# Optimization experiments

Measured on AMD Instinct MI355X. Metric: run time of the kernel, lower is better.

The kernel has to match this reference:

```python
import jax, jax.numpy as jnp
import numpy as np

S, B, L, V, D, T, G = 16, 8, 8, 32000, 1024, 512, 3


def setup_inputs() -> dict:
    key = jax.random.key(0)
    k = jax.random.split(key, 10)
    s = 0.05
    return {
        "encoded_hidden": jax.random.normal(k[0], (B, D), jnp.float32),
        "encoded_outputs": jax.random.normal(k[1], (B, T, D), jnp.float32),
        "story": jax.random.randint(k[2], (B, T), 0, V),
        "trg_batches": jax.random.randint(k[3], (B, S, L), 0, V),
        "embedding": jax.random.normal(k[4], (V, D), jnp.float32) * 0.1,
        "w_ih": jax.random.normal(k[5], (3 * D, D), jnp.float32) * s,
        "w_hh": jax.random.normal(k[6], (3 * D, D), jnp.float32) * s,
        "b_ih": jnp.zeros((3 * D,), jnp.float32),
        "b_hh": jnp.zeros((3 * D,), jnp.float32),
        "w_ratio_w": jax.random.normal(k[7], (1, 3 * D), jnp.float32) * s,
        "w_ratio_b": jnp.zeros((1,), jnp.float32),
        "w_gate_w": jax.random.normal(k[8], (G, D), jnp.float32) * s,
        "w_gate_b": jnp.zeros((G,), jnp.float32),
        "slot_emb": jax.random.normal(k[9], (S, D), jnp.float32) * 0.1,
    }


def reference(encoded_hidden, encoded_outputs, story, trg_batches, embedding,
              w_ih, w_hh, b_ih, b_hh, w_ratio_w, w_ratio_b,
              w_gate_w, w_gate_b, slot_emb):
    # Decoder inputs per (slot, step): step 0 = slot embedding,
    # step i>0 = embedding of teacher-forced target token i-1.  -> x: (S,L,B,D)
    x0 = jnp.broadcast_to(slot_emb[:, None, None, :], (S, 1, B, D))
    xt = jnp.transpose(embedding[trg_batches[:, :, :L - 1]], (1, 2, 0, 3))  # (S,L-1,B,D)
    x = jnp.concatenate([x0, xt], axis=1)

    # Single GRU step; hidden is reset to the encoder hidden each step (as in source),
    # so decoder_state == new hidden and all (slot,step) cells are independent.
    h0 = encoded_hidden  # (B,D)
    gi = jnp.einsum('slbd,ed->slbe', x, w_ih) + b_ih          # (S,L,B,3D)
    gh = h0 @ w_hh.T + b_hh                                    # (B,3D)
    ir, iz, inn = jnp.split(gi, 3, axis=-1)
    hr, hz, hn = jnp.split(gh, 3, axis=-1)
    r = jax.nn.sigmoid(ir + hr)
    z = jax.nn.sigmoid(iz + hz)
    n = jnp.tanh(inn + r * hn)
    h = (1.0 - z) * n + z * h0                                 # (S,L,B,D)

    # History attention; NOTE: context uses the RAW scores (source quirk).
    scores = jnp.einsum('slbd,btd->slbt', h, encoded_outputs)  # (S,L,B,T)
    probs = jax.nn.softmax(scores, axis=-1)
    context = jnp.einsum('slbt,btd->slbd', scores, encoded_outputs)

    # Vocab distribution p_vocab = softmax(h @ E^T)
    p_vocab = jax.nn.softmax(jnp.einsum('slbd,vd->slbv', h, embedding), axis=-1)

    # Pointer-generator gate
    feat = jnp.concatenate([h, context, x], axis=-1)           # (S,L,B,3D)
    p_gen = jax.nn.sigmoid(jnp.einsum('slbe,oe->slbo', feat, w_ratio_w) + w_ratio_b)  # (S,L,B,1)

    # Copy distribution via scatter-add of attention probs onto vocab ids
    def scatter_one(p_b, story_b):  # p_b: (S,L,T), story_b: (T,)
        return jnp.zeros((S, L, V), p_b.dtype).at[:, :, story_b].add(p_b)
    p_ctx = jax.vmap(scatter_one, in_axes=(2, 0), out_axes=2)(probs, story)  # (S,L,B,V)

    p_final = p_gen * p_vocab + (1.0 - p_gen) * p_ctx
    ptr_outputs = jnp.transpose(p_final, (0, 2, 1, 3))         # (S,B,L,V)
    gate_outputs = context[:, 0] @ w_gate_w.T + w_gate_b       # (S,B,G), from step 0
    return ptr_outputs, gate_outputs
```

## Files before the change

### kernel.cpp

```cpp
#include <hip/hip_runtime.h>

#define S_ 16
#define B_ 8
#define L_ 8
#define V_ 32000
#define D_ 1024
#define T_ 512
#define G_ 3
#define M_ 1024
#define E3_ 3072

typedef unsigned short U16;
typedef __attribute__((ext_vector_type(8))) short short8;
typedef __attribute__((ext_vector_type(4))) float f32x4;

__device__ __forceinline__ U16 f2bf(float f) {
  union { float f; unsigned u; } c; c.f = f;
  unsigned u = c.u;
  return (U16)((u + 0x7FFFu + ((u >> 16) & 1u)) >> 16);
}
__device__ __forceinline__ float bf2f(U16 h) {
  union { unsigned u; float f; } c; c.u = ((unsigned)h) << 16;
  return c.f;
}
__device__ __forceinline__ void split2(float f, U16& hi, U16& lo) {
  hi = f2bf(f);
  lo = f2bf(f - bf2f(hi));
}

__global__ void k_cast_emb(const float* __restrict__ emb, U16* __restrict__ emb_bf) {
  int idx = blockIdx.x * 256 + threadIdx.x;
  float4 v = ((const float4*)emb)[idx];
  ushort4 o;
  o.x = f2bf(v.x); o.y = f2bf(v.y); o.z = f2bf(v.z); o.w = f2bf(v.w);
  ((ushort4*)emb_bf)[idx] = o;
}

__global__ void k_cast_wih(const float* __restrict__ w, U16* __restrict__ wh, U16* __restrict__ wl) {
  int idx = blockIdx.x * 256 + threadIdx.x;
  float4 v = ((const float4*)w)[idx];
  ushort4 h4, l4;
  split2(v.x, h4.x, l4.x); split2(v.y, h4.y, l4.y);
  split2(v.z, h4.z, l4.z); split2(v.w, h4.w, l4.w);
  ((ushort4*)wh)[idx] = h4;
  ((ushort4*)wl)[idx] = l4;
}

__global__ void k_cast_enc(const float* __restrict__ enc,
                           U16* __restrict__ enc_h, U16* __restrict__ enc_l,
                           U16* __restrict__ encT_h, U16* __restrict__ encT_l) {
  __shared__ U16 hs[32][36];
  __shared__ U16 ls[32][36];
  int b = blockIdx.z, t0 = blockIdx.x * 32, d0 = blockIdx.y * 32;
  int r  = threadIdx.x >> 3;
  int c4 = (threadIdx.x & 7) * 4;
  size_t src_idx = ((size_t)(b * T_ + t0 + r)) * D_ + d0 + c4;
  float4 v = *(const float4*)(enc + src_idx);
  ushort4 h4, l4;
  split2(v.x, h4.x, l4.x); split2(v.y, h4.y, l4.y);
  split2(v.z, h4.z, l4.z); split2(v.w, h4.w, l4.w);
  *(ushort4*)(enc_h + src_idx) = h4;
  *(ushort4*)(enc_l + src_idx) = l4;
  hs[r][c4+0] = h4.x; hs[r][c4+1] = h4.y; hs[r][c4+2] = h4.z; hs[r][c4+3] = h4.w;
  ls[r][c4+0] = l4.x; ls[r][c4+1] = l4.y; ls[r][c4+2] = l4.z; ls[r][c4+3] = l4.w;
  __syncthreads();
  ushort4 th, tl;
  th.x = hs[c4+0][r]; th.y = hs[c4+1][r]; th.z = hs[c4+2][r]; th.w = hs[c4+3][r];
  tl.x = ls[c4+0][r]; tl.y = ls[c4+1][r]; tl.z = ls[c4+2][r]; tl.w = ls[c4+3][r];
  size_t dst_idx = ((size_t)(b * D_ + d0 + r)) * T_ + t0 + c4;
  *(ushort4*)(encT_h + dst_idx) = th;
  *(ushort4*)(encT_l + dst_idx) = tl;
}

__global__ void k_build_x(const float* __restrict__ emb, const float* __restrict__ slot_emb,
                          const int* __restrict__ trg, float* __restrict__ x,
                          U16* __restrict__ x_h, U16* __restrict__ x_l) {
  int m = blockIdx.x;
  int d = threadIdx.x * 4;
  int b = m >> 7, s = (m >> 3) & 15, l = m & 7;
  const float* src;
  if (l == 0) src = slot_emb + s * D_;
  else        src = emb + (size_t)trg[b * (S_ * L_) + s * L_ + (l - 1)] * D_;
  float4 v = *(const float4*)(src + d);
  *(float4*)(x + (size_t)m * D_ + d) = v;
  ushort4 h4, l4;
  split2(v.x, h4.x, l4.x); split2(v.y, h4.y, l4.y);
  split2(v.z, h4.z, l4.z); split2(v.w, h4.w, l4.w);
  *(ushort4*)(x_h + (size_t)m * D_ + d) = h4;
  *(ushort4*)(x_l + (size_t)m * D_ + d) = l4;
}

__global__ void k_gh(const float* __restrict__ h0, const float* __restrict__ w_hh,
                     const float* __restrict__ b_hh, float* __restrict__ gh) {
  int b = blockIdx.y;
  int e = blockIdx.x * 64 + (threadIdx.x >> 2);
  int part = threadIdx.x & 3;
  const float* hr = h0 + b * D_ + part * 256;
  const float* wr = w_hh + (size_t)e * D_ + part * 256;
  float s = 0.f;
  for (int i = 0; i < 256; ++i) s += hr[i] * wr[i];
  s += __shfl_xor(s, 1);
  s += __shfl_xor(s, 2);
  if (part == 0) gh[b * E3_ + e] = s + b_hh[e];
}

__device__ __forceinline__ void stage_tile(U16* __restrict__ sm, const U16* __restrict__ g,
                                           int row0, int k0, int lda, int tid) {
#pragma unroll
  for (int i = 0; i < 2; ++i) {
    int o = (i * 256 + tid) * 16;
    int row = o >> 6;
    int chunk = ((o >> 4) & 3) ^ ((row >> 1) & 3);
    const U16* gp = g + (size_t)(row0 + row) * lda + k0 + chunk * 8;
    U16* sp = sm + (o >> 1);
    __builtin_amdgcn_global_load_lds((const __attribute__((address_space(1))) unsigned int*)gp,
                                     (__attribute__((address_space(3))) unsigned int*)sp,
                                     16, 0, 0);
  }
}

__device__ __forceinline__ short8 frag_ld(const U16* __restrict__ sm, int rowbase, int ln) {
  int row = rowbase + (ln & 15);
  int chunk = (ln >> 4) ^ ((row >> 1) & 3);
  return *(const short8*)(sm + row * 32 + chunk * 8);
}

template <bool HILO, bool VOCAB>
__global__ __launch_bounds__(256, 2)
void k_gemm(const U16* __restrict__ Ah, const U16* __restrict__ Al,
            const U16* __restrict__ Bh, const U16* __restrict__ Bl,
            float* __restrict__ C, float* __restrict__ rowsum,
            int Ktot, int lda, int ldb, int ldc,
            long sA, long sB, long sC) {
  __shared__ U16 smem[(HILO ? 4 : 2) * 128 * 32];
  U16* Ash = smem;
  U16* Bsh = smem + 4096;
  U16* Asl = HILO ? (smem + 8192) : smem;
  U16* Bsl = HILO ? (smem + 12288) : smem;

  int tid = threadIdx.x;
  int ln = tid & 63, w = tid >> 6;
  int wr = (w >> 1) * 64, wc = (w & 1) * 64;
  int n0 = blockIdx.x * 128, m0 = blockIdx.y * 128;
  int bz = blockIdx.z;
  const U16* pAh = Ah + (size_t)bz * sA;
  const U16* pBh = Bh + (size_t)bz * sB;
  const U16* pAl = HILO ? (Al + (size_t)bz * sA) : nullptr;
  const U16* pBl = HILO ? (Bl + (size_t)bz * sB) : nullptr;

  f32x4 acc[4][4];
#pragma unroll
  for (int i = 0; i < 4; i++)
#pragma unroll
    for (int j = 0; j < 4; j++) acc[i][j] = (f32x4)(0.f);

  for (int k0 = 0; k0 < Ktot; k0 += 32) {
    __syncthreads();
    stage_tile(Ash, pAh, m0, k0, lda, tid);
    stage_tile(Bsh, pBh, n0, k0, ldb, tid);
    if constexpr (HILO) {
      stage_tile(Asl, pAl, m0, k0, lda, tid);
      stage_tile(Bsl, pBl, n0, k0, ldb, tid);
    }
    __syncthreads();

    short8 a_h[4], b_h[4];
#pragma unroll
    for (int i = 0; i < 4; i++) {
      a_h[i] = frag_ld(Ash, wr + i * 16, ln);
      b_h[i] = frag_ld(Bsh, wc + i * 16, ln);
    }
    if constexpr (HILO) {
      short8 a_l[4], b_l[4];
#pragma unroll
      for (int i = 0; i < 4; i++) {
        a_l[i] = frag_ld(Asl, wr + i * 16, ln);
        b_l[i] = frag_ld(Bsl, wc + i * 16, ln);
      }
#pragma unroll
      for (int i = 0; i < 4; i++)
#pragma unroll
        for (int j = 0; j < 4; j++) {
          acc[i][j] = __builtin_amdgcn_mfma_f32_16x16x32_bf16(a_h[i], b_h[j], acc[i][j], 0, 0, 0);
          acc[i][j] = __builtin_amdgcn_mfma_f32_16x16x32_bf16(a_h[i], b_l[j], acc[i][j], 0, 0, 0);
          acc[i][j] = __builtin_amdgcn_mfma_f32_16x16x32_bf16(a_l[i], b_h[j], acc[i][j], 0, 0, 0);
        }
    } else {
#pragma unroll
      for (int i = 0; i < 4; i++)
#pragma unroll
        for (int j = 0; j < 4; j++)
          acc[i][j] = __builtin_amdgcn_mfma_f32_16x16x32_bf16(a_h[i], b_h[j], acc[i][j], 0, 0, 0);
    }
  }

  int quad = ln >> 4, col = ln & 15;
  if constexpr (!VOCAB) {
    float* pC = C + (size_t)bz * sC;
#pragma unroll
    for (int i = 0; i < 4; i++)
#pragma unroll
      for (int j = 0; j < 4; j++)
#pragma unroll
        for (int r = 0; r < 4; r++)
          pC[(size_t)(m0 + wr + i * 16 + quad * 4 + r) * ldc + (n0 + wc + j * 16 + col)] =
              acc[i][j][r];
  } else {
#pragma unroll
    for (int i = 0; i < 4; i++)
#pragma unroll
      for (int r = 0; r < 4; r++) {
        int m = m0 + wr + i * 16 + quad * 4 + r;
        int s_ = (m >> 3) & 15, l_ = m & 7, b_ = m >> 7;
        size_t obase = (size_t)((s_ * B_ + b_) * L_ + l_) * (size_t)V_;
        float rs = 0.f;
#pragma unroll
        for (int j = 0; j < 4; j++) {
          float e = __expf(acc[i][j][r]);
          C[obase + (n0 + wc + j * 16 + col)] = e;
          rs += e;
        }
        rs += __shfl_xor(rs, 1);
        rs += __shfl_xor(rs, 2);
        rs += __shfl_xor(rs, 4);
        rs += __shfl_xor(rs, 8);
        if (col == 0) atomicAdd(&rowsum[m], rs);
      }
  }
}

__global__ void k_h(const float* __restrict__ gi, const float* __restrict__ gh,
                    const float* __restrict__ h0, const float* __restrict__ b_ih,
                    float* __restrict__ h, U16* __restrict__ h_h, U16* __restrict__ h_l) {
  int m = blockIdx.x;
  int d = threadIdx.x * 4;
  int b = m >> 7;
  float4 ir  = *(const float4*)(gi + (size_t)m * E3_ + d);
  float4 iz  = *(const float4*)(gi + (size_t)m * E3_ + D_ + d);
  float4 in_ = *(const float4*)(gi + (size_t)m * E3_ + 2 * D_ + d);
  float4 bir = *(const float4*)(b_ih + d);
  float4 biz = *(const float4*)(b_ih + D_ + d);
  float4 bin = *(const float4*)(b_ih + 2 * D_ + d);
  float4 hr  = *(const float4*)(gh + b * E3_ + d);
  float4 hz  = *(const float4*)(gh + b * E3_ + D_ + d);
  float4 hn  = *(const float4*)(gh + b * E3_ + 2 * D_ + d);
  float4 h0v = *(const float4*)(h0 + b * D_ + d);
  float4 out;
#define GRU1(c)                                             \
  {                                                         \
    float rr = 1.f / (1.f + __expf(-(ir.c + bir.c + hr.c))); \
    float zz = 1.f / (1.f + __expf(-(iz.c + biz.c + hz.c))); \
    float nn = tanhf(in_.c + bin.c + rr * hn.c);            \
    out.c = (1.f - zz) * nn + zz * h0v.c;                   \
  }
  GRU1(x) GRU1(y) GRU1(z) GRU1(w)
#undef GRU1
  *(float4*)(h + (size_t)m * D_ + d) = out;
  ushort4 h4, l4;
  split2(out.x, h4.x, l4.x); split2(out.y, h4.y, l4.y);
  split2(out.z, h4.z, l4.z); split2(out.w, h4.w, l4.w);
  *(ushort4*)(h_h + (size_t)m * D_ + d) = h4;
  *(ushort4*)(h_l + (size_t)m * D_ + d) = l4;
}

__global__ void k_softmax(const float* __restrict__ scores, float* __restrict__ probs,
                          U16* __restrict__ s_h, U16* __restrict__ s_l) {
  int m = blockIdx.x;
  int tid = threadIdx.x;
  int ln = tid & 63, w = tid >> 6;
  float v0 = scores[(size_t)m * T_ + tid];
  float v1 = scores[(size_t)m * T_ + 256 + tid];
  U16 hh, ll;
  split2(v0, hh, ll); s_h[m * T_ + tid] = hh;       s_l[m * T_ + tid] = ll;
  split2(v1, hh, ll); s_h[m * T_ + 256 + tid] = hh; s_l[m * T_ + 256 + tid] = ll;
  float mx = fmaxf(v0, v1);
#pragma unroll
  for (int msk = 32; msk >= 1; msk >>= 1) mx = fmaxf(mx, __shfl_xor(mx, msk));
  __shared__ float red[4];
  if (ln == 0) red[w] = mx;
  __syncthreads();
  mx = fmaxf(fmaxf(red[0], red[1]), fmaxf(red[2], red[3]));
  float e0 = __expf(v0 - mx), e1 = __expf(v1 - mx);
  float sm = e0 + e1;
#pragma unroll
  for (int msk = 32; msk >= 1; msk >>= 1) sm += __shfl_xor(sm, msk);
  __syncthreads();
  if (ln == 0) red[w] = sm;
  __syncthreads();
  float inv = 1.f / (red[0] + red[1] + red[2] + red[3]);
  probs[(size_t)m * T_ + tid] = e0 * inv;
  probs[(size_t)m * T_ + 256 + tid] = e1 * inv;
}

__global__ void k_pgen(const float* __restrict__ h, const float* __restrict__ ctx,
                       const float* __restrict__ x, const float* __restrict__ wr,
                       const float* __restrict__ wrb, float* __restrict__ p_gen,
                       float* __restrict__ rowsum) {
  int m = blockIdx.x;
  int tid = threadIdx.x;
  int ln = tid & 63, w = tid >> 6;
  float sacc = 0.f;
  for (int j = tid; j < D_; j += 256)
    sacc += h[(size_t)m * D_ + j] * wr[j] + ctx[(size_t)m * D_ + j] * wr[D_ + j] +
            x[(size_t)m * D_ + j] * wr[2 * D_ + j];
#pragma unroll
  for (int msk = 32; msk >= 1; msk >>= 1) sacc += __shfl_xor(sacc, msk);
  __shared__ float red[4];
  if (ln == 0) red[w] = sacc;
  __syncthreads();
  if (tid == 0) {
    float t = red[0] + red[1] + red[2] + red[3] + wrb[0];
    p_gen[m] = 1.f / (1.f + expf(-t));
    rowsum[m] = 0.f;
  }
}

__global__ void k_gate(const float* __restrict__ ctx, const float* __restrict__ wg,
                       const float* __restrict__ wgb, float* __restrict__ out_gate) {
  int id = blockIdx.x;
  int g = id % 3;
  int sb = id / 3;
  int b = sb & 7, s = sb >> 3;
  int m = (b * S_ + s) * L_;
  int ln = threadIdx.x;
  float acc = 0.f;
  for (int d = ln; d < D_; d += 64) acc += ctx[(size_t)m * D_ + d] * wg[g * D_ + d];
#pragma unroll
  for (int msk = 32; msk >= 1; msk >>= 1) acc += __shfl_xor(acc, msk);
  if (ln == 0) out_gate[id] = acc + wgb[g];
}

__global__ void k_scale(float* __restrict__ out, const float* __restrict__ p_gen,
                        const float* __restrict__ rowsum) {
  int idx = blockIdx.x * 256 + threadIdx.x;
  int osl = idx / (V_ / 4);
  int s = osl >> 6, b = (osl >> 3) & 7, l = osl & 7;
  int m = (b << 7) | (s << 3) | l;
  float sc = p_gen[m] / rowsum[m];
  float4* p = (float4*)out + idx;
  float4 v = *p;
  v.x *= sc; v.y *= sc; v.z *= sc; v.w *= sc;
  *p = v;
}

__global__ void k_scatter(float* __restrict__ out, const float* __restrict__ p_gen,
                          const float* __restrict__ probs, const int* __restrict__ story) {
  int id = blockIdx.x * 256 + threadIdx.x;
  int m = id >> 9, t = id & 511;
  int b = m >> 7, s = (m >> 3) & 15, l = m & 7;
  float val = (1.f - p_gen[m]) * probs[(size_t)m * T_ + t];
  int v = story[b * T_ + t];
  size_t o = (size_t)((s * B_ + b) * L_ + l) * (size_t)V_ + v;
  atomicAdd(out + o, val);
}

extern "C" void kernel_launch(void* const* d_in, const int* in_sizes, int n_in,
                              void* d_out, int out_size, void* d_ws, size_t ws_size,
                              hipStream_t stream) {
  (void)in_sizes; (void)n_in; (void)out_size; (void)ws_size;
  const float* enc_hid   = (const float*)d_in[0];
  const float* enc_out   = (const float*)d_in[1];
  const int*   story     = (const int*)d_in[2];
  const int*   trg       = (const int*)d_in[3];
  const float* emb       = (const float*)d_in[4];
  const float* w_ih      = (const float*)d_in[5];
  const float* w_hh      = (const float*)d_in[6];
  const float* b_ih      = (const float*)d_in[7];
  const float* b_hh      = (const float*)d_in[8];
  const float* w_ratio_w = (const float*)d_in[9];
  const float* w_ratio_b = (const float*)d_in[10];
  const float* w_gate_w  = (const float*)d_in[11];
  const float* w_gate_b  = (const float*)d_in[12];
  const float* slot_emb  = (const float*)d_in[13];
  float* out = (float*)d_out;

  char* ws = (char*)d_ws;
  size_t off = 0;
  auto alloc = [&](size_t bytes) -> void* {
    void* p = ws + off;
    off += (bytes + 255) & ~(size_t)255;
    return p;
  };
  U16* emb_bf   = (U16*)alloc((size_t)V_ * D_ * 2);
  float* x      = (float*)alloc((size_t)M_ * D_ * 4);
  U16* x_h      = (U16*)alloc((size_t)M_ * D_ * 2);
  U16* x_l      = (U16*)alloc((size_t)M_ * D_ * 2);
  U16* wih_h    = (U16*)alloc((size_t)E3_ * D_ * 2);
  U16* wih_l    = (U16*)alloc((size_t)E3_ * D_ * 2);
  U16* enc_h    = (U16*)alloc((size_t)B_ * T_ * D_ * 2);
  U16* enc_l    = (U16*)alloc((size_t)B_ * T_ * D_ * 2);
  U16* encT_h   = (U16*)alloc((size_t)B_ * T_ * D_ * 2);
  U16* encT_l   = (U16*)alloc((size_t)B_ * T_ * D_ * 2);
  float* gh     = (float*)alloc((size_t)B_ * E3_ * 4);
  float* gi     = (float*)alloc((size_t)M_ * E3_ * 4);
  float* h      = (float*)alloc((size_t)M_ * D_ * 4);
  U16* h_h      = (U16*)alloc((size_t)M_ * D_ * 2);
  U16* h_l      = (U16*)alloc((size_t)M_ * D_ * 2);
  float* scores = (float*)alloc((size_t)M_ * T_ * 4);
  U16* sc_h     = (U16*)alloc((size_t)M_ * T_ * 2);
  U16* sc_l     = (U16*)alloc((size_t)M_ * T_ * 2);
  float* probs  = (float*)alloc((size_t)M_ * T_ * 4);
  float* ctx    = (float*)alloc((size_t)M_ * D_ * 4);
  float* p_gen  = (float*)alloc((size_t)M_ * 4);
  float* rowsum = (float*)alloc((size_t)M_ * 4);

  k_cast_emb<<<V_ * D_ / 4 / 256, 256, 0, stream>>>(emb, emb_bf);
  k_cast_wih<<<E3_ * D_ / 4 / 256, 256, 0, stream>>>(w_ih, wih_h, wih_l);
  k_cast_enc<<<dim3(T_ / 32, D_ / 32, B_), 256, 0, stream>>>(enc_out, enc_h, enc_l, encT_h, encT_l);
  k_build_x<<<M_, 256, 0, stream>>>(emb, slot_emb, trg, x, x_h, x_l);
  k_gh<<<dim3(E3_ / 64, B_), 256, 0, stream>>>(enc_hid, w_hh, b_hh, gh);

  k_gemm<true, false><<<dim3(E3_ / 128, M_ / 128, 1), 256, 0, stream>>>(
      x_h, x_l, wih_h, wih_l, gi, nullptr, D_, D_, D_, E3_, 0, 0, 0);

  k_h<<<M_, 256, 0, stream>>>(gi, gh, enc_hid, b_ih, h, h_h, h_l);

  k_gemm<true, false><<<dim3(T_ / 128, 1, B_), 256, 0, stream>>>(
      h_h, h_l, enc_h, enc_l, scores, nullptr, D_, D_, D_, T_,
      (long)(S_ * L_) * D_, (long)T_ * D_, (long)(S_ * L_) * T_);

  k_softmax<<<M_, 256, 0, stream>>>(scores, probs, sc_h, sc_l);

  k_gemm<true, false><<<dim3(D_ / 128, 1, B_), 256, 0, stream>>>(
      sc_h, sc_l, encT_h, encT_l, ctx, nullptr, T_, T_, T_, D_,
      (long)(S_ * L_) * T_, (long)D_ * T_, (long)(S_ * L_) * D_);

  k_pgen<<<M_, 256, 0, stream>>>(h, ctx, x, w_ratio_w, w_ratio_b, p_gen, rowsum);
  k_gate<<<S_ * B_ * G_, 64, 0, stream>>>(ctx, w_gate_w, w_gate_b, out + (size_t)M_ * V_);

  k_gemm<false, true><<<dim3(V_ / 128, M_ / 128, 1), 256, 0, stream>>>(
      h_h, nullptr, emb_bf, nullptr, out, rowsum, D_, D_, D_, V_, 0, 0, 0);

  k_scale<<<M_ * V_ / 4 / 256, 256, 0, stream>>>(out, p_gen, rowsum);
  k_scatter<<<M_ * T_ / 256, 256, 0, stream>>>(out, p_gen, probs, story);
}
```

Measured before the change: 672.9 us.

## Retile vocab GEMM with BK=64, swapped grid, and per-tile partial row sums

The vocab GEMM now uses a 64-wide K tile with a matching 8-chunk XOR swizzle. The grid is swapped so consecutive blocks share the same embedding tile, which should improve L2 reuse of the large B matrix. Global atomics on the row sums are replaced by a shared-memory reduction that writes per-tile partials. A per-row scale kernel then reduces those partials and rescales the row. This removes contended global atomics and the rowsum reset, at the cost of an extra partial buffer and larger shared memory per block.

Measured after the change: 593.7 us. -11.8%, faster.

```diff
diff --git a/kernel.cpp b/kernel.cpp
--- a/kernel.cpp
+++ b/kernel.cpp
@@ -9,6 +9,7 @@
 #define G_ 3
 #define M_ 1024
 #define E3_ 3072
+#define NT_ 250
 
 typedef unsigned short U16;
 typedef __attribute__((ext_vector_type(8))) short short8;
@@ -104,14 +105,22 @@
   if (part == 0) gh[b * E3_ + e] = s + b_hh[e];
 }
 
+template <int BK>
 __device__ __forceinline__ void stage_tile(U16* __restrict__ sm, const U16* __restrict__ g,
                                            int row0, int k0, int lda, int tid) {
-#pragma unroll
-  for (int i = 0; i < 2; ++i) {
+  constexpr int PASSES = (128 * BK * 2) / 4096;
+#pragma unroll
+  for (int i = 0; i < PASSES; ++i) {
     int o = (i * 256 + tid) * 16;
-    int row = o >> 6;
-    int chunk = ((o >> 4) & 3) ^ ((row >> 1) & 3);
-    const U16* gp = g + (size_t)(row0 + row) * lda + k0 + chunk * 8;
+    int row, gc;
+    if constexpr (BK == 32) {
+      row = o >> 6;
+      gc = ((o >> 4) & 3) ^ ((row >> 1) & 3);
+    } else {
+      row = o >> 7;
+      gc = ((o >> 4) & 7) ^ (row & 7);
+    }
+    const U16* gp = g + (size_t)(row0 + row) * lda + k0 + gc * 8;
     U16* sp = sm + (o >> 1);
     __builtin_amdgcn_global_load_lds((const __attribute__((address_space(1))) unsigned int*)gp,
                                      (__attribute__((address_space(3))) unsigned int*)sp,
@@ -119,78 +128,95 @@
   }
 }
 
-__device__ __forceinline__ short8 frag_ld(const U16* __restrict__ sm, int rowbase, int ln) {
+template <int BK>
+__device__ __forceinline__ short8 frag_ld(const U16* __restrict__ sm, int rowbase, int ln, int kh) {
   int row = rowbase + (ln & 15);
-  int chunk = (ln >> 4) ^ ((row >> 1) & 3);
-  return *(const short8*)(sm + row * 32 + chunk * 8);
-}
-
-template <bool HILO, bool VOCAB>
+  if constexpr (BK == 32) {
+    int c = (ln >> 4) ^ ((row >> 1) & 3);
+    return *(const short8*)(sm + row * 32 + c * 8);
+  } else {
+    int c = (kh * 4 + (ln >> 4)) ^ (row & 7);
+    return *(const short8*)(sm + row * 64 + c * 8);
+  }
+}
+
+template <int BK, bool HILO, bool VOCAB, bool SWAP>
 __global__ __launch_bounds__(256, 2)
 void k_gemm(const U16* __restrict__ Ah, const U16* __restrict__ Al,
             const U16* __restrict__ Bh, const U16* __restrict__ Bl,
-            float* __restrict__ C, float* __restrict__ rowsum,
+            float* __restrict__ C, float* __restrict__ part,
             int Ktot, int lda, int ldb, int ldc,
             long sA, long sB, long sC) {
-  __shared__ U16 smem[(HILO ? 4 : 2) * 128 * 32];
+  constexpr int TILE_U16 = 128 * BK;
+  __shared__ U16 smem[(HILO ? 4 : 2) * TILE_U16];
+  __shared__ float rsred[128];
   U16* Ash = smem;
-  U16* Bsh = smem + 4096;
-  U16* Asl = HILO ? (smem + 8192) : smem;
-  U16* Bsl = HILO ? (smem + 12288) : smem;
+  U16* Bsh = smem + TILE_U16;
+  U16* Asl = HILO ? (smem + 2 * TILE_U16) : smem;
+  U16* Bsl = HILO ? (smem + 3 * TILE_U16) : smem;
 
   int tid = threadIdx.x;
   int ln = tid & 63, w = tid >> 6;
   int wr = (w >> 1) * 64, wc = (w & 1) * 64;
-  int n0 = blockIdx.x * 128, m0 = blockIdx.y * 128;
+  int m0 = (SWAP ? blockIdx.x : blockIdx.y) * 128;
+  int n0 = (SWAP ? blockIdx.y : blockIdx.x) * 128;
+  int ntile = SWAP ? blockIdx.y : blockIdx.x;
   int bz = blockIdx.z;
   const U16* pAh = Ah + (size_t)bz * sA;
   const U16* pBh = Bh + (size_t)bz * sB;
   const U16* pAl = HILO ? (Al + (size_t)bz * sA) : nullptr;
   const U16* pBl = HILO ? (Bl + (size_t)bz * sB) : nullptr;
 
+  if constexpr (VOCAB) {
+    if (tid < 128) rsred[tid] = 0.f;
+  }
+
   f32x4 acc[4][4];
 #pragma unroll
   for (int i = 0; i < 4; i++)
 #pragma unroll
     for (int j = 0; j < 4; j++) acc[i][j] = (f32x4)(0.f);
 
-  for (int k0 = 0; k0 < Ktot; k0 += 32) {
+  for (int k0 = 0; k0 < Ktot; k0 += BK) {
     __syncthreads();
-    stage_tile(Ash, pAh, m0, k0, lda, tid);
-    stage_tile(Bsh, pBh, n0, k0, ldb, tid);
+    stage_tile<BK>(Ash, pAh, m0, k0, lda, tid);
+    stage_tile<BK>(Bsh, pBh, n0, k0, ldb, tid);
     if constexpr (HILO) {
-      stage_tile(Asl, pAl, m0, k0, lda, tid);
-      stage_tile(Bsl, pBl, n0, k0, ldb, tid);
+      stage_tile<BK>(Asl, pAl, m0, k0, lda, tid);
+      stage_tile<BK>(Bsl, pBl, n0, k0, ldb, tid);
     }
     __syncthreads();
 
-    short8 a_h[4], b_h[4];
-#pragma unroll
-    for (int i = 0; i < 4; i++) {
-      a_h[i] = frag_ld(Ash, wr + i * 16, ln);
-      b_h[i] = frag_ld(Bsh, wc + i * 16, ln);
-    }
-    if constexpr (HILO) {
-      short8 a_l[4], b_l[4];
+#pragma unroll
+    for (int kh = 0; kh < BK / 32; kh++) {
+      short8 a_h[4], b_h[4];
 #pragma unroll
       for (int i = 0; i < 4; i++) {
-        a_l[i] = frag_ld(Asl, wr + i * 16, ln);
-        b_l[i] = frag_ld(Bsl, wc + i * 16, ln);
+        a_h[i] = frag_ld<BK>(Ash, wr + i * 16, ln, kh);
+        b_h[i] = frag_ld<BK>(Bsh, wc + i * 16, ln, kh);
       }
-#pragma unroll
-      for (int i = 0; i < 4; i++)
-#pragma unroll
-        for (int j = 0; j < 4; j++) {
-          acc[i][j] = __builtin_amdgcn_mfma_f32_16x16x32_bf16(a_h[i], b_h[j], acc[i][j], 0, 0, 0);
-          acc[i][j] = __builtin_amdgcn_mfma_f32_16x16x32_bf16(a_h[i], b_l[j], acc[i][j], 0, 0, 0);
-          acc[i][j] = __builtin_amdgcn_mfma_f32_16x16x32_bf16(a_l[i], b_h[j], acc[i][j], 0, 0, 0);
+      if constexpr (HILO) {
+        short8 a_l[4], b_l[4];
+#pragma unroll
+        for (int i = 0; i < 4; i++) {
+          a_l[i] = frag_ld<BK>(Asl, wr + i * 16, ln, kh);
+          b_l[i] = frag_ld<BK>(Bsl, wc + i * 16, ln, kh);
         }
-    } else {
-#pragma unroll
-      for (int i = 0; i < 4; i++)
-#pragma unroll
-        for (int j = 0; j < 4; j++)
-          acc[i][j] = __builtin_amdgcn_mfma_f32_16x16x32_bf16(a_h[i], b_h[j], acc[i][j], 0, 0, 0);
+#pragma unroll
+        for (int i = 0; i < 4; i++)
+#pragma unroll
+          for (int j = 0; j < 4; j++) {
+            acc[i][j] = __builtin_amdgcn_mfma_f32_16x16x32_bf16(a_h[i], b_h[j], acc[i][j], 0, 0, 0);
+            acc[i][j] = __builtin_amdgcn_mfma_f32_16x16x32_bf16(a_h[i], b_l[j], acc[i][j], 0, 0, 0);
+            acc[i][j] = __builtin_amdgcn_mfma_f32_16x16x32_bf16(a_l[i], b_h[j], acc[i][j], 0, 0, 0);
+          }
+      } else {
+#pragma unroll
+        for (int i = 0; i < 4; i++)
+#pragma unroll
+          for (int j = 0; j < 4; j++)
+            acc[i][j] = __builtin_amdgcn_mfma_f32_16x16x32_bf16(a_h[i], b_h[j], acc[i][j], 0, 0, 0);
+      }
     }
   }
 
@@ -224,8 +250,10 @@
         rs += __shfl_xor(rs, 2);
         rs += __shfl_xor(rs, 4);
         rs += __shfl_xor(rs, 8);
-        if (col == 0) atomicAdd(&rowsum[m], rs);
+        if (col == 0) atomicAdd(&rsred[(wr + i * 16 + quad * 4 + r)], rs);
       }
+    __syncthreads();
+    if (tid < 128) part[(size_t)ntile * M_ + (m0 + tid)] = rsred[tid];
   }
 }
 
@@ -294,8 +322,7 @@
 
 __global__ void k_pgen(const float* __restrict__ h, const float* __restrict__ ctx,
                        const float* __restrict__ x, const float* __restrict__ wr,
-                       const float* __restrict__ wrb, float* __restrict__ p_gen,
-                       float* __restrict__ rowsum) {
+                       const float* __restrict__ wrb, float* __restrict__ p_gen) {
   int m = blockIdx.x;
   int tid = threadIdx.x;
   int ln = tid & 63, w = tid >> 6;
@@ -311,7 +338,6 @@
   if (tid == 0) {
     float t = red[0] + red[1] + red[2] + red[3] + wrb[0];
     p_gen[m] = 1.f / (1.f + expf(-t));
-    rowsum[m] = 0.f;
   }
 }
 
@@ -331,16 +357,26 @@
 }
 
 __global__ void k_scale(float* __restrict__ out, const float* __restrict__ p_gen,
-                        const float* __restrict__ rowsum) {
-  int idx = blockIdx.x * 256 + threadIdx.x;
-  int osl = idx / (V_ / 4);
-  int s = osl >> 6, b = (osl >> 3) & 7, l = osl & 7;
-  int m = (b << 7) | (s << 3) | l;
-  float sc = p_gen[m] / rowsum[m];
-  float4* p = (float4*)out + idx;
-  float4 v = *p;
-  v.x *= sc; v.y *= sc; v.z *= sc; v.w *= sc;
-  *p = v;
+                        const float* __restrict__ part) {
+  int m = blockIdx.x;
+  int tid = threadIdx.x, ln = tid & 63, w = tid >> 6;
+  float ps = (tid < NT_) ? part[(size_t)tid * M_ + m] : 0.f;
+#pragma unroll
+  for (int msk = 32; msk >= 1; msk >>= 1) ps += __shfl_xor(ps, msk);
+  __shared__ float red[4];
+  __shared__ float scs;
+  if (ln == 0) red[w] = ps;
+  __syncthreads();
+  if (tid == 0) scs = p_gen[m] / (red[0] + red[1] + red[2] + red[3]);
+  __syncthreads();
+  float sc = scs;
+  int b = m >> 7, s = (m >> 3) & 15, l = m & 7;
+  float4* p = (float4*)(out + (size_t)((s * B_ + b) * L_ + l) * (size_t)V_);
+  for (int j = tid; j < V_ / 4; j += 256) {
+    float4 v = p[j];
+    v.x *= sc; v.y *= sc; v.z *= sc; v.w *= sc;
+    p[j] = v;
+  }
 }
 
 __global__ void k_scatter(float* __restrict__ out, const float* __restrict__ p_gen,
@@ -402,7 +438,7 @@
   float* probs  = (float*)alloc((size_t)M_ * T_ * 4);
   float* ctx    = (float*)alloc((size_t)M_ * D_ * 4);
   float* p_gen  = (float*)alloc((size_t)M_ * 4);
-  float* rowsum = (float*)alloc((size_t)M_ * 4);
+  float* part   = (float*)alloc((size_t)NT_ * M_ * 4);
 
   k_cast_emb<<<V_ * D_ / 4 / 256, 256, 0, stream>>>(emb, emb_bf);
   k_cast_wih<<<E3_ * D_ / 4 / 256, 256, 0, stream>>>(w_ih, wih_h, wih_l);
@@ -410,27 +446,27 @@
   k_build_x<<<M_, 256, 0, stream>>>(emb, slot_emb, trg, x, x_h, x_l);
   k_gh<<<dim3(E3_ / 64, B_), 256, 0, stream>>>(enc_hid, w_hh, b_hh, gh);
 
-  k_gemm<true, false><<<dim3(E3_ / 128, M_ / 128, 1), 256, 0, stream>>>(
+  k_gemm<32, true, false, false><<<dim3(E3_ / 128, M_ / 128, 1), 256, 0, stream>>>(
       x_h, x_l, wih_h, wih_l, gi, nullptr, D_, D_, D_, E3_, 0, 0, 0);
 
   k_h<<<M_, 256, 0, stream>>>(gi, gh, enc_hid, b_ih, h, h_h, h_l);
 
-  k_gemm<true, false><<<dim3(T_ / 128, 1, B_), 256, 0, stream>>>(
+  k_gemm<32, true, false, false><<<dim3(T_ / 128, 1, B_), 256, 0, stream>>>(
       h_h, h_l, enc_h, enc_l, scores, nullptr, D_, D_, D_, T_,
       (long)(S_ * L_) * D_, (long)T_ * D_, (long)(S_ * L_) * T_);
 
   k_softmax<<<M_, 256, 0, stream>>>(scores, probs, sc_h, sc_l);
 
-  k_gemm<true, false><<<dim3(D_ / 128, 1, B_), 256, 0, stream>>>(
+  k_gemm<32, true, false, false><<<dim3(D_ / 128, 1, B_), 256, 0, stream>>>(
       sc_h, sc_l, encT_h, encT_l, ctx, nullptr, T_, T_, T_, D_,
       (long)(S_ * L_) * T_, (long)D_ * T_, (long)(S_ * L_) * D_);
 
-  k_pgen<<<M_, 256, 0, stream>>>(h, ctx, x, w_ratio_w, w_ratio_b, p_gen, rowsum);
+  k_pgen<<<M_, 256, 0, stream>>>(h, ctx, x, w_ratio_w, w_ratio_b, p_gen);
   k_gate<<<S_ * B_ * G_, 64, 0, stream>>>(ctx, w_gate_w, w_gate_b, out + (size_t)M_ * V_);
 
-  k_gemm<false, true><<<dim3(V_ / 128, M_ / 128, 1), 256, 0, stream>>>(
-      h_h, nullptr, emb_bf, nullptr, out, rowsum, D_, D_, D_, V_, 0, 0, 0);
-
-  k_scale<<<M_ * V_ / 4 / 256, 256, 0, stream>>>(out, p_gen, rowsum);
+  k_gemm<64, false, true, true><<<dim3(M_ / 128, V_ / 128, 1), 256, 0, stream>>>(
+      h_h, nullptr, emb_bf, nullptr, out, part, D_, D_, D_, V_, 0, 0, 0);
+
+  k_scale<<<M_, 256, 0, stream>>>(out, p_gen, part);
   k_scatter<<<M_ * T_ / 256, 256, 0, stream>>>(out, p_gen, probs, story);
 }
```
